# Optimization experiments

Measured on AMD Instinct MI355X. Metric: run time of the kernel, lower is better.

The kernel has to match this reference:

```python
import jax, jax.numpy as jnp
from jax import lax
import numpy as np

N = 4096   # layer_size
R = 4      # displacement rank
B = 8192   # batch
STD = 0.01 # init_stddev


def setup_inputs() -> dict:
    key = jax.random.key(0)
    k1, k2, k3 = jax.random.split(key, 3)
    x = jax.random.normal(k1, (B, N), jnp.float32)
    G = jax.random.normal(k2, (R, N), jnp.float32) * STD
    H = jax.random.normal(k3, (R, N), jnp.float32) * STD
    return {"x": x, "G": G, "H": H}


def _krylov(f, V, n):
    """Krylov matrices K(Z_f, v_i) for each row v_i of V: (r, n) -> (r, n, n).
    Z_f is the shift-down matrix with corner f: (Z_f v)[0] = f*v[n-1], (Z_f v)[j] = v[j-1].
    Column k of the output is Z_f^k v_i."""
    def step(c, _):
        nxt = jnp.concatenate([f * c[:, -1:], c[:, :-1]], axis=1)
        return nxt, c
    _, cols = lax.scan(step, V, None, length=n)  # (n, r, n): k-th slice is Z_f^k V
    return jnp.transpose(cols, (1, 2, 0))        # (r, n, k)


def reference(x, G, H):
    n = G.shape[1]
    KA = _krylov(1.0, G, n)    # fn_A   = Z_mult_fn(1)
    KB = _krylov(-1.0, H, n)   # fn_B_T = Z_mult_fn(-1)
    # Stein reconstruction: W - Z_1 W Z_{-1}^T... summed series; Z_1^n = I, Z_{-1}^n = -I => factor 1/2
    W = 0.5 * jnp.einsum('rik,rjk->ij', KA, KB)  # (n, n)
    return x @ W.T
```

## Files before the change

### kernel.cpp

```cpp
#include <hip/hip_runtime.h>
#include <hip/hip_bf16.h>

#define NN 4096
#define RR 4
#define BB 8192
#define CHUNK 64
#define NCHUNK (NN / CHUNK)

typedef __bf16 bf16x8 __attribute__((ext_vector_type(8)));
typedef float f32x4 __attribute__((ext_vector_type(4)));
typedef unsigned short u16;
typedef unsigned int u32;

#define GLOBAL_AS(p) ((const __attribute__((address_space(1))) u32*)(p))
#define LDS_AS(p) ((__attribute__((address_space(3))) u32*)(p))

__device__ inline u32 pack_bf2(float lo, float hi) {
    __hip_bfloat162 h2 = __float22bfloat162_rn(make_float2(lo, hi));
    return *(u32*)&h2;
}

__global__ __launch_bounds__(256) void cast_x_kernel(const float* __restrict__ x,
                                                     u16* __restrict__ xbf) {
    size_t i = (size_t)blockIdx.x * 256 + threadIdx.x;
    const float4* x4 = (const float4*)x;
    float4 a = x4[i * 2], b = x4[i * 2 + 1];
    uint4 o = make_uint4(pack_bf2(a.x, a.y), pack_bf2(a.z, a.w),
                         pack_bf2(b.x, b.y), pack_bf2(b.z, b.w));
    *(uint4*)(xbf + i * 8) = o;
}

__global__ void ksum_kernel(const float* __restrict__ G, const float* __restrict__ H,
                            float* __restrict__ S_T) {
    int dblk = blockIdx.x & 15;
    int J = blockIdx.x >> 4;
    int d = dblk * 256 + threadIdx.x;
    int t0 = J * CHUNK;
    float acc = 0.f;
#pragma unroll 4
    for (int tt = 0; tt < CHUNK; ++tt) {
        int t = t0 + tt;
        float h0 = H[t], h1 = H[NN + t], h2 = H[2 * NN + t], h3 = H[3 * NN + t];
        int idx = (d + t) & (NN - 1);
        acc += G[idx] * h0 + G[NN + idx] * h1 + G[2 * NN + idx] * h2 + G[3 * NN + idx] * h3;
    }
    S_T[J * NN + d] = acc;
}

__global__ __launch_bounds__(128) void kprefix_kernel(const float* __restrict__ G,
                                                      const float* __restrict__ H,
                                                      const float* __restrict__ S_T,
                                                      u16* __restrict__ W) {
    __shared__ u32 tile32[64 * 33];
    u16* tile = (u16*)tile32;

    int itile = blockIdx.x >> 6;
    int J = blockIdx.x & 63;
    int i0 = itile * 64, t0 = J * CHUNK;
    int dl = threadIdx.x;
    int d = (i0 - t0 - 63 + dl) & (NN - 1);

    float pre = 0.f, tot = 0.f;
    for (int Jp = 0; Jp < NCHUNK; ++Jp) {
        float v = S_T[Jp * NN + d];
        if (Jp < J) pre += v;
        tot += v;
    }
    float acc = pre - 0.5f * tot;

#pragma unroll 4
    for (int tt = 0; tt < CHUNK; ++tt) {
        int t = t0 + tt;
        float h0 = H[t], h1 = H[NN + t], h2 = H[2 * NN + t], h3 = H[3 * NN + t];
        int idx = (d + t) & (NN - 1);
        acc += G[idx] * h0 + G[NN + idx] * h1 + G[2 * NN + idx] * h2 + G[3 * NN + idx] * h3;
        int r = dl + tt - 63;
        if ((unsigned)r < 64u) {
            __hip_bfloat16 w = __float2bfloat16(acc);
            tile[r * 66 + tt] = *(u16*)&w;
        }
    }
    __syncthreads();

    int r = threadIdx.x >> 3;
    int c8 = threadIdx.x & 7;
#pragma unroll
    for (int pass = 0; pass < 4; ++pass) {
        int rr = pass * 16 + r;
        const u32* s = &tile32[rr * 33 + c8 * 4];
        uint4 v = make_uint4(s[0], s[1], s[2], s[3]);
        *(uint4*)(W + (size_t)(i0 + rr) * NN + t0 + c8 * 8) = v;
    }
}


#define ST_A(kt, c) do { \
    const u16* s_ = srcA + (size_t)(c) * (64 * NN) + (size_t)(kt) * 64; \
    char* d_ = (char*)As + (((kt) & 1) * 32768) + ((c) * 8192) + t16; \
    __builtin_amdgcn_global_load_lds(GLOBAL_AS(s_), LDS_AS(d_), 16, 0, 0); \
    __builtin_amdgcn_global_load_lds(GLOBAL_AS(s_ + (size_t)128 * NN), LDS_AS(d_ + 16384), 16, 0, 0); \
} while (0)

#define ST_B(kt, hb) do { \
    const u16* s_ = srcB + (size_t)(hb) * (128 * NN) + (size_t)(kt) * 64; \
    char* d_ = (char*)Bs + (((kt) & 1) * 32768) + ((hb) * 16384) + t16; \
    __builtin_amdgcn_global_load_lds(GLOBAL_AS(s_), LDS_AS(d_), 16, 0, 0); \
    __builtin_amdgcn_global_load_lds(GLOBAL_AS(s_ + (size_t)64 * NN), LDS_AS(d_ + 8192), 16, 0, 0); \
} while (0)

#define AFR(cp, mi, ks) (*(const bf16x8*)(Abase + (cp) * 32768 + (mi) * 2048 + (sx ^ ((ks) << 6))))
#define BFR(cp, ni, ks) (*(const bf16x8*)(Bbase + (cp) * 32768 + (ni) * 2048 + (sx ^ ((ks) << 6))))

#define MM2(mi, ni, A0, A1) do { \
    acc[mi][ni] = __builtin_amdgcn_mfma_f32_16x16x32_bf16(A0, bq[2 * (ni)], acc[mi][ni], 0, 0, 0); \
    acc[mi][ni] = __builtin_amdgcn_mfma_f32_16x16x32_bf16(A1, bq[2 * (ni) + 1], acc[mi][ni], 0, 0, 0); \
} while (0)

#define PH(cp, mp, STAGES, WAITC) do { \
    bf16x8 xa0 = AFR(cp, mp, 0), xa1 = AFR(cp, mp, 1); \
    bf16x8 xa2 = AFR(cp, (mp) + 1, 0), xa3 = AFR(cp, (mp) + 1, 1); \
    if ((mp) == 0) { \
        bq[0] = BFR(cp, 0, 0); bq[1] = BFR(cp, 0, 1); \
        bq[2] = BFR(cp, 1, 0); bq[3] = BFR(cp, 1, 1); \
        bq[4] = BFR(cp, 2, 0); bq[5] = BFR(cp, 2, 1); \
        bq[6] = BFR(cp, 3, 0); bq[7] = BFR(cp, 3, 1); \
    } \
    STAGES; \
    WAITC; \
    __builtin_amdgcn_s_barrier(); \
    asm volatile("s_waitcnt lgkmcnt(0)" ::: "memory"); \
    __builtin_amdgcn_sched_barrier(0); \
    __builtin_amdgcn_s_setprio(1); \
    MM2(mp, 0, xa0, xa1); MM2(mp, 1, xa0, xa1); \
    MM2(mp, 2, xa0, xa1); MM2(mp, 3, xa0, xa1); \
    MM2((mp) + 1, 0, xa2, xa3); MM2((mp) + 1, 1, xa2, xa3); \
    MM2((mp) + 1, 2, xa2, xa3); MM2((mp) + 1, 3, xa2, xa3); \
    __builtin_amdgcn_s_setprio(0); \
    __builtin_amdgcn_s_barrier(); \
} while (0)

__global__ __launch_bounds__(512, 2) void gemm256_kernel(const u16* __restrict__ At,
                                                         const u16* __restrict__ Bt,
                                                         float* __restrict__ C) {
    __shared__ __align__(16) u16 As[2][2][2][64][64];
    __shared__ __align__(16) u16 Bs[2][2][2][64][64];

    int bid = blockIdx.x;
    int swz = (bid & 7) * 64 + (bid >> 3);
    int bx = swz & 15, by = swz >> 4;
    int m0 = by * 256, n0 = bx * 256;

    int t = threadIdx.x;
    int lane = t & 63, wave = t >> 6;
    int wm = wave >> 2, wn = wave & 3;
    int lrow = lane & 15, lq = lane >> 4;

    int rowt = t >> 3;
    int colel = ((t & 7) ^ (rowt & 7)) << 3;
    const u16* srcA = At + (size_t)(m0 + rowt) * NN + colel;
    const u16* srcB = Bt + (size_t)(n0 + rowt) * NN + colel;
    int t16 = t * 16;

    const char* Abase = (const char*)As + wm * 16384 + lrow * 128;
    const char* Bbase = (const char*)Bs + (wn >> 1) * 16384 + (wn & 1) * 8192 + lrow * 128;
    int sx = (lq << 4) ^ ((lrow & 7) << 4);

    f32x4 acc[8][4] = {};
    bf16x8 bq[8];

    ST_B(0, 0); ST_B(0, 1); ST_A(0, 0); ST_A(0, 1);
    ST_B(1, 0); ST_B(1, 1); ST_A(1, 0);
    asm volatile("s_waitcnt vmcnt(6)" ::: "memory");
    __builtin_amdgcn_s_barrier();

#pragma unroll 1
    for (int i = 0; i < 31; ++i) {
        int k0 = 2 * i;
        PH(0, 0, ST_A(k0 + 1, 1), );
        PH(0, 2, ST_B(k0 + 2, 0), );
        PH(0, 4, ST_B(k0 + 2, 1), );
        PH(0, 6, ST_A(k0 + 2, 0), asm volatile("s_waitcnt vmcnt(6)" ::: "memory"));
        PH(1, 0, ST_A(k0 + 2, 1), );
        PH(1, 2, ST_B(k0 + 3, 0), );
        PH(1, 4, ST_B(k0 + 3, 1), );
        PH(1, 6, ST_A(k0 + 3, 0), asm volatile("s_waitcnt vmcnt(6)" ::: "memory"));
    }
    PH(0, 0, ST_A(63, 1), );
    PH(0, 2, , );
    PH(0, 4, , );
    PH(0, 6, , asm volatile("s_waitcnt vmcnt(0)" ::: "memory"));
    PH(1, 0, , );
    PH(1, 2, , );
    PH(1, 4, , );
    PH(1, 6, , );

#pragma unroll
    for (int mi = 0; mi < 8; ++mi)
#pragma unroll
        for (int ni = 0; ni < 4; ++ni)
#pragma unroll
            for (int e = 0; e < 4; ++e) {
                int row = m0 + wm * 128 + mi * 16 + lq * 4 + e;
                int col = n0 + wn * 64 + ni * 16 + lrow;
                C[(size_t)row * NN + col] = acc[mi][ni][e];
            }
}

extern "C" void kernel_launch(void* const* d_in, const int* in_sizes, int n_in,
                              void* d_out, int out_size, void* d_ws, size_t ws_size,
                              hipStream_t stream) {
    const float* x = (const float*)d_in[0];
    const float* G = (const float*)d_in[1];
    const float* H = (const float*)d_in[2];
    float* y = (float*)d_out;

    char* ws = (char*)d_ws;
    u16* xbf = (u16*)ws;
    u16* Wbf = (u16*)(ws + (size_t)BB * NN * 2);
    float* S_T = (float*)(ws + (size_t)BB * NN * 2 + (size_t)NN * NN * 2);

    hipLaunchKernelGGL(cast_x_kernel, dim3((size_t)BB * NN / 8 / 256), dim3(256), 0, stream,
                       x, xbf);
    hipLaunchKernelGGL(ksum_kernel, dim3((NN / 256) * NCHUNK), dim3(256), 0, stream, G, H, S_T);
    hipLaunchKernelGGL(kprefix_kernel, dim3(64 * 64), dim3(128), 0, stream, G, H, S_T, Wbf);
    hipLaunchKernelGGL(gemm256_kernel, dim3((BB / 256) * (NN / 256)), dim3(512), 0, stream,
                       xbf, Wbf, y);
}
```

Before: 480.7 us.

## Double-buffer LDS fragment registers to overlap ds_reads with MFMA in GEMM

Restructures the GEMM main loop so A and B fragments for the next phase are read from LDS into alternate register sets while the current phase's MFMAs run. Partial lgkmcnt waits replace the full drain before each MFMA block. The intent is to hide LDS read latency behind matrix math. In exchange it raises VGPR pressure, which may hurt occupancy at 512 threads with two blocks per CU, and it relies on the barrier ordering to keep the prefetched reads from racing the global-to-LDS staging.

```diff
diff --git a/kernel.cpp b/kernel.cpp
--- a/kernel.cpp
+++ b/kernel.cpp
@@ -111,32 +111,47 @@
 #define AFR(cp, mi, ks) (*(const bf16x8*)(Abase + (cp) * 32768 + (mi) * 2048 + (sx ^ ((ks) << 6))))
 #define BFR(cp, ni, ks) (*(const bf16x8*)(Bbase + (cp) * 32768 + (ni) * 2048 + (sx ^ ((ks) << 6))))
 
-#define MM2(mi, ni, A0, A1) do { \
-    acc[mi][ni] = __builtin_amdgcn_mfma_f32_16x16x32_bf16(A0, bq[2 * (ni)], acc[mi][ni], 0, 0, 0); \
-    acc[mi][ni] = __builtin_amdgcn_mfma_f32_16x16x32_bf16(A1, bq[2 * (ni) + 1], acc[mi][ni], 0, 0, 0); \
-} while (0)
-
-#define PH(cp, mp, STAGES, WAITC) do { \
-    bf16x8 xa0 = AFR(cp, mp, 0), xa1 = AFR(cp, mp, 1); \
-    bf16x8 xa2 = AFR(cp, (mp) + 1, 0), xa3 = AFR(cp, (mp) + 1, 1); \
-    if ((mp) == 0) { \
-        bq[0] = BFR(cp, 0, 0); bq[1] = BFR(cp, 0, 1); \
-        bq[2] = BFR(cp, 1, 0); bq[3] = BFR(cp, 1, 1); \
-        bq[4] = BFR(cp, 2, 0); bq[5] = BFR(cp, 2, 1); \
-        bq[6] = BFR(cp, 3, 0); bq[7] = BFR(cp, 3, 1); \
-    } \
+#define LDXA(XA, cp, mp) do { \
+    XA[0] = AFR(cp, mp, 0); XA[1] = AFR(cp, mp, 1); \
+    XA[2] = AFR(cp, (mp) + 1, 0); XA[3] = AFR(cp, (mp) + 1, 1); \
+} while (0)
+
+#define LDBQ(BQ, cp) do { \
+    BQ[0] = BFR(cp, 0, 0); BQ[1] = BFR(cp, 0, 1); \
+    BQ[2] = BFR(cp, 1, 0); BQ[3] = BFR(cp, 1, 1); \
+    BQ[4] = BFR(cp, 2, 0); BQ[5] = BFR(cp, 2, 1); \
+    BQ[6] = BFR(cp, 3, 0); BQ[7] = BFR(cp, 3, 1); \
+} while (0)
+
+#define MFMA_(a, b, c) __builtin_amdgcn_mfma_f32_16x16x32_bf16(a, b, c, 0, 0, 0)
+
+#define MM1(mi, ni, A0, A1, BQ) do { \
+    acc[mi][ni] = MFMA_(A0, BQ[2 * (ni)], acc[mi][ni]); \
+    acc[mi][ni] = MFMA_(A1, BQ[2 * (ni) + 1], acc[mi][ni]); \
+} while (0)
+
+#define MMQ(mp, XA, BQ) do { \
+    MM1(mp, 0, XA[0], XA[1], BQ); MM1(mp, 1, XA[0], XA[1], BQ); \
+    MM1(mp, 2, XA[0], XA[1], BQ); MM1(mp, 3, XA[0], XA[1], BQ); \
+    MM1((mp) + 1, 0, XA[2], XA[3], BQ); MM1((mp) + 1, 1, XA[2], XA[3], BQ); \
+    MM1((mp) + 1, 2, XA[2], XA[3], BQ); MM1((mp) + 1, 3, XA[2], XA[3], BQ); \
+} while (0)
+
+#define VMC(n) asm volatile("s_waitcnt vmcnt(" #n ")" ::: "memory")
+
+#define PH_BODY(mp, XAc, BQc, RA, NLG, STAGES, WAITC) do { \
     STAGES; \
     WAITC; \
     __builtin_amdgcn_s_barrier(); \
-    asm volatile("s_waitcnt lgkmcnt(0)" ::: "memory"); \
+    __builtin_amdgcn_sched_barrier(0); \
+    RA; \
+    asm volatile("s_waitcnt lgkmcnt(" NLG ")" ::: "memory"); \
     __builtin_amdgcn_sched_barrier(0); \
     __builtin_amdgcn_s_setprio(1); \
-    MM2(mp, 0, xa0, xa1); MM2(mp, 1, xa0, xa1); \
-    MM2(mp, 2, xa0, xa1); MM2(mp, 3, xa0, xa1); \
-    MM2((mp) + 1, 0, xa2, xa3); MM2((mp) + 1, 1, xa2, xa3); \
-    MM2((mp) + 1, 2, xa2, xa3); MM2((mp) + 1, 3, xa2, xa3); \
+    MMQ(mp, XAc, BQc); \
     __builtin_amdgcn_s_setprio(0); \
     __builtin_amdgcn_s_barrier(); \
+    __builtin_amdgcn_sched_barrier(0); \
 } while (0)
 
 __global__ __launch_bounds__(512, 2) void gemm256_kernel(const u16* __restrict__ At,
@@ -166,33 +181,38 @@
     int sx = (lq << 4) ^ ((lrow & 7) << 4);
 
     f32x4 acc[8][4] = {};
-    bf16x8 bq[8];
+    bf16x8 xa0[4], xa1[4], bq0[8], bq1[8];
 
     ST_B(0, 0); ST_B(0, 1); ST_A(0, 0); ST_A(0, 1);
     ST_B(1, 0); ST_B(1, 1); ST_A(1, 0);
-    asm volatile("s_waitcnt vmcnt(6)" ::: "memory");
+    VMC(6);
     __builtin_amdgcn_s_barrier();
+    __builtin_amdgcn_sched_barrier(0);
+    LDBQ(bq0, 0);
+    LDXA(xa0, 0, 0);
 
 #pragma unroll 1
     for (int i = 0; i < 31; ++i) {
         int k0 = 2 * i;
-        PH(0, 0, ST_A(k0 + 1, 1), );
-        PH(0, 2, ST_B(k0 + 2, 0), );
-        PH(0, 4, ST_B(k0 + 2, 1), );
-        PH(0, 6, ST_A(k0 + 2, 0), asm volatile("s_waitcnt vmcnt(6)" ::: "memory"));
-        PH(1, 0, ST_A(k0 + 2, 1), );
-        PH(1, 2, ST_B(k0 + 3, 0), );
-        PH(1, 4, ST_B(k0 + 3, 1), );
-        PH(1, 6, ST_A(k0 + 3, 0), asm volatile("s_waitcnt vmcnt(6)" ::: "memory"));
-    }
-    PH(0, 0, ST_A(63, 1), );
-    PH(0, 2, , );
-    PH(0, 4, , );
-    PH(0, 6, , asm volatile("s_waitcnt vmcnt(0)" ::: "memory"));
-    PH(1, 0, , );
-    PH(1, 2, , );
-    PH(1, 4, , );
-    PH(1, 6, , );
+        PH_BODY(0, xa0, bq0, LDXA(xa1, 0, 2), "4", ST_A(k0 + 1, 1), );
+        PH_BODY(2, xa1, bq0, LDXA(xa0, 0, 4), "4", ST_B(k0 + 2, 0), );
+        PH_BODY(4, xa0, bq0, LDXA(xa1, 0, 6), "4", ST_B(k0 + 2, 1), );
+        PH_BODY(6, xa1, bq0, { LDBQ(bq1, 1); LDXA(xa0, 1, 0); }, "12",
+                ST_A(k0 + 2, 0), VMC(6));
+        PH_BODY(0, xa0, bq1, LDXA(xa1, 1, 2), "4", ST_A(k0 + 2, 1), );
+        PH_BODY(2, xa1, bq1, LDXA(xa0, 1, 4), "4", ST_B(k0 + 3, 0), );
+        PH_BODY(4, xa0, bq1, LDXA(xa1, 1, 6), "4", ST_B(k0 + 3, 1), );
+        PH_BODY(6, xa1, bq1, { LDBQ(bq0, 0); LDXA(xa0, 0, 0); }, "12",
+                ST_A(k0 + 3, 0), VMC(6));
+    }
+    PH_BODY(0, xa0, bq0, LDXA(xa1, 0, 2), "4", ST_A(63, 1), );
+    PH_BODY(2, xa1, bq0, LDXA(xa0, 0, 4), "4", , );
+    PH_BODY(4, xa0, bq0, LDXA(xa1, 0, 6), "4", , );
+    PH_BODY(6, xa1, bq0, { LDBQ(bq1, 1); LDXA(xa0, 1, 0); }, "12", , VMC(0));
+    PH_BODY(0, xa0, bq1, LDXA(xa1, 1, 2), "4", , );
+    PH_BODY(2, xa1, bq1, LDXA(xa0, 1, 4), "4", , );
+    PH_BODY(4, xa0, bq1, LDXA(xa1, 1, 6), "4", , );
+    PH_BODY(6, xa1, bq1, , "0", , );
 
 #pragma unroll
     for (int mi = 0; mi < 8; ++mi)
```

After: 498.8 us. 1.04x slower.
